# Kernel optimization log

Hardware: AMD Instinct MI355X
Metric: run time of the kernel (lower is better)

The kernel has to match this reference:

```python
import jax, jax.numpy as jnp
import numpy as np

H = 16  # heads

def setup_inputs() -> dict:
    key = jax.random.key(0)
    k1, k2, k3 = jax.random.split(key, 3)
    B, N, D = 2, 2048, 1024
    x = jax.random.normal(k1, (B, N, D), dtype=jnp.float32)
    W1 = jax.random.normal(k2, (D, 3 * D), dtype=jnp.float32) * (1.0 / np.sqrt(D))
    b1 = jnp.zeros((3 * D,), dtype=jnp.float32)
    W2 = jax.random.normal(k3, (D, D), dtype=jnp.float32) * (1.0 / np.sqrt(D))
    b2 = jnp.zeros((D,), dtype=jnp.float32)
    return {"x": x, "W1": W1, "b1": b1, "W2": W2, "b2": b2}

def reference(x, W1, b1, W2, b2):
    B, N, D = x.shape
    Dh = D // H  # head dim
    qkv = x @ W1 + b1                         # [B,N,3D]
    q, k, v = jnp.split(qkv, 3, axis=-1)
    q = q.reshape(B, N, H, Dh).transpose(0, 2, 1, 3)  # [B,H,N,Dh]
    k = k.reshape(B, N, H, Dh).transpose(0, 2, 1, 3)
    v = v.reshape(B, N, H, Dh).transpose(0, 2, 1, 3)
    scale = 1.0 / np.sqrt(Dh)
    w = jnp.einsum('bhnd,bhmd->bhnm', q, k) * scale   # [B,H,N,N]
    w = jax.nn.softmax(w, axis=-1)
    out = jnp.einsum('bhnm,bhmd->bhnd', w, v)         # [B,H,N,Dh]
    out = out.transpose(0, 2, 1, 3).reshape(B, N, D)
    return out @ W2 + b2
```

## Files before the change

kernel.cpp:

```cpp
#include <hip/hip_runtime.h>
#include <hip/hip_bf16.h>
#include <stdint.h>

#define B_   2
#define H_   16
#define N_   2048
#define D_   1024
#define DH   64
#define MTOK 4096

#define LOG2E 1.44269504088896f

typedef __attribute__((ext_vector_type(8)))  short bf16x8;
typedef __attribute__((ext_vector_type(4)))  float f32x4;
typedef __attribute__((ext_vector_type(16))) float f32x16;
typedef __attribute__((ext_vector_type(2)))  unsigned u32x2;
typedef __attribute__((ext_vector_type(4)))  unsigned short us4;

#define VMCNT_ASM(N) asm volatile("s_waitcnt vmcnt(" #N ")" ::: "memory")

static __device__ __forceinline__ unsigned short f2bf(float f) {
    union { float f; unsigned u; } v; v.f = f;
    unsigned r = v.u + 0x7fffu + ((v.u >> 16) & 1u);
    return (unsigned short)(r >> 16);
}

static __device__ __forceinline__ unsigned f2u(float x) {
    union { float f; unsigned u; } v; v.f = x; return v.u;
}
static __device__ __forceinline__ float u2f(unsigned x) {
    union { unsigned u; float f; } v; v.u = x; return v.f;
}

static __device__ __forceinline__ unsigned cvt_pk_bf16(float lo, float hi) {
    unsigned r;
    asm("v_cvt_pk_bf16_f32 %0, %1, %2" : "=v"(r) : "v"(lo), "v"(hi));
    return r;
}

static __device__ __forceinline__ bf16x8 frag_from_u32(unsigned a, unsigned b, unsigned c, unsigned d) {
    union { unsigned u[4]; bf16x8 v; } x;
    x.u[0] = a; x.u[1] = b; x.u[2] = c; x.u[3] = d;
    return x.v;
}

static __device__ __forceinline__ void load_lds16(const void* g, void* l) {
    __builtin_amdgcn_global_load_lds(
        (const __attribute__((address_space(1))) unsigned int*)g,
        (__attribute__((address_space(3))) unsigned int*)l, 16, 0, 0);
}

__global__ __launch_bounds__(256) void k_pre(const float* __restrict__ x,
                                             unsigned short* __restrict__ xb,
                                             const float* __restrict__ W1,
                                             unsigned short* __restrict__ w1t,
                                             const float* __restrict__ W2,
                                             unsigned short* __restrict__ w2t) {
    int blk = blockIdx.x;
    int t = threadIdx.x;
    if (blk < 4096) {
        int idx = (blk * 256 + t) * 4;
        float4 v = *(const float4*)(x + idx);
        us4 o;
        o.x = f2bf(v.x); o.y = f2bf(v.y); o.z = f2bf(v.z); o.w = f2bf(v.w);
        *(us4*)(xb + idx) = o;
        return;
    }
    const float* in;
    unsigned short* out;
    int C, bx, by;
    if (blk < 4864) { in = W1; out = w1t; C = 3072; int b2 = blk - 4096; bx = b2 % 48; by = b2 / 48; }
    else            { in = W2; out = w2t; C = 1024; int b2 = blk - 4864; bx = b2 % 16; by = b2 / 16; }
    const int R = 1024;
    __shared__ float tile[64][65];
    int c0 = bx * 64, r0 = by * 64;
    int tr = t >> 4, tc = (t & 15) * 4;
#pragma unroll
    for (int p = 0; p < 4; p++) {
        int row = p * 16 + tr;
        float4 v = *(const float4*)(in + (size_t)(r0 + row) * C + c0 + tc);
        tile[row][tc + 0] = v.x; tile[row][tc + 1] = v.y;
        tile[row][tc + 2] = v.z; tile[row][tc + 3] = v.w;
    }
    __syncthreads();
    int oc = t >> 4, orr = (t & 15) * 4;
#pragma unroll
    for (int p = 0; p < 4; p++) {
        int crow = p * 16 + oc;
        us4 o;
        o.x = f2bf(tile[orr + 0][crow]);
        o.y = f2bf(tile[orr + 1][crow]);
        o.z = f2bf(tile[orr + 2][crow]);
        o.w = f2bf(tile[orr + 3][crow]);
        *(us4*)(out + (size_t)(c0 + crow) * R + r0 + orr) = o;
    }
}

__global__ __launch_bounds__(512, 2) void k_gemm0(const unsigned short* __restrict__ A,
                                                  const unsigned short* __restrict__ Bt,
                                                  const float* __restrict__ bias,
                                                  unsigned short* __restrict__ qdst,
                                                  unsigned short* __restrict__ kdst,
                                                  unsigned short* __restrict__ vdst) {
    __shared__ unsigned short lds[57344];
    const int K = 1024, NT = 16;
    int tid = threadIdx.x;
    int lane = tid & 63, wv = tid >> 6;
    int wm = wv >> 2, wn = wv & 3;
    int F = blockIdx.x;
    int L = (F & 7) * 32 + (F >> 3);
    int n0 = (L % 16) * 192;
    int m0 = (L / 16) * 256;

    f32x4 acc[8][3];
#pragma unroll
    for (int i = 0; i < 8; i++)
#pragma unroll
        for (int j = 0; j < 3; j++) {
            f32x4 z; z[0] = 0.f; z[1] = 0.f; z[2] = 0.f; z[3] = 0.f;
            acc[i][j] = z;
        }

    auto stage = [&](int t) {
        int p = t & 1;
        int k0 = t * 64;
        unsigned short* ab = &lds[p * 16384];
        unsigned short* bb = &lds[32768 + p * 12288];
#pragma unroll
        for (int i = 0; i < 4; i++) {
            int u = i * 512 + tid;
            int r = u >> 3, c8 = u & 7;
            int c8s = c8 ^ (r & 7);
            int db = (i * 512 + wv * 64) * 8;
            load_lds16(A + (size_t)(m0 + r) * K + k0 + c8s * 8, &ab[db]);
            if (i < 3)
                load_lds16(Bt + (size_t)(n0 + r) * K + k0 + c8s * 8, &bb[db]);
        }
    };

    stage(0);
    stage(1);

    const int ml = lane & 15, ul = lane >> 4;
    bf16x8 afr[4], bfr[3];

#pragma unroll 1
    for (int t = 0; t < NT; ++t) {
        if (t < NT - 1) { VMCNT_ASM(7); }
        else            { VMCNT_ASM(0); }
        __builtin_amdgcn_s_barrier();

        const unsigned short* ab = &lds[(t & 1) * 16384];
        const unsigned short* bb = &lds[32768 + (t & 1) * 12288];

#pragma unroll
        for (int kk = 0; kk < 2; ++kk) {
            int ck = ((kk * 4 + ul) ^ (ml & 7)) * 8;
#pragma unroll
            for (int mh = 0; mh < 2; ++mh) {
                if (mh == 0) {
#pragma unroll
                    for (int nj = 0; nj < 3; nj++)
                        bfr[nj] = *(const bf16x8*)&bb[(wn * 48 + nj * 16 + ml) * 64 + ck];
                }
#pragma unroll
                for (int q = 0; q < 4; q++)
                    afr[q] = *(const bf16x8*)&ab[(wm * 128 + (mh * 4 + q) * 16 + ml) * 64 + ck];
                __builtin_amdgcn_s_barrier();
                __builtin_amdgcn_s_setprio(1);
#pragma unroll
                for (int q = 0; q < 4; q++)
#pragma unroll
                    for (int nj = 0; nj < 3; nj++)
                        acc[mh * 4 + q][nj] = __builtin_amdgcn_mfma_f32_16x16x32_bf16(
                            afr[q], bfr[nj], acc[mh * 4 + q][nj], 0, 0, 0);
                __builtin_amdgcn_s_setprio(0);
                __builtin_amdgcn_s_barrier();
            }
        }
        if (t + 2 < NT) stage(t + 2);
    }

#pragma unroll
    for (int nj = 0; nj < 3; nj++) {
        int col = n0 + wn * 48 + nj * 16 + (lane & 15);
        float bv = bias[col];
        int which = col >> 10;
        int hd = (col >> 6) & 15;
        int dh = col & 63;
        float scl = (which == 0) ? (0.125f * LOG2E) : 1.0f;
#pragma unroll
        for (int mi = 0; mi < 8; mi++) {
            int rbase = m0 + wm * 128 + mi * 16 + (lane >> 4) * 4;
#pragma unroll
            for (int r = 0; r < 4; r++) {
                int tok = rbase + r;
                int bb2 = tok >> 11, nn = tok & 2047;
                float vvv = (acc[mi][nj][r] + bv) * scl;
                size_t chunk = ((size_t)(bb2 * H_ + hd) * 64 + (nn >> 5)) * 2048;
                if (which == 0) {
                    qdst[((size_t)(bb2 * H_ + hd) * N_ + nn) * DH + dh] = f2bf(vvv);
                } else if (which == 1) {
                    int lane2 = ((dh >> 3) & 1) * 32 + (nn & 31);
                    kdst[chunk + (dh >> 4) * 512 + lane2 * 8 + (dh & 7)] = f2bf(vvv);
                } else {
                    int lane2 = ((nn >> 3) & 1) * 32 + (dh & 31);
                    int islot = (dh >> 5) * 2 + ((nn >> 4) & 1);
                    vdst[chunk + islot * 512 + lane2 * 8 + (nn & 7)] = f2bf(vvv);
                }
            }
        }
    }
}

__global__ __launch_bounds__(512, 2) void k_gemm1(const unsigned short* __restrict__ A,
                                                  const unsigned short* __restrict__ Bt,
                                                  const float* __restrict__ bias,
                                                  float* __restrict__ outp) {
    __shared__ unsigned short lds1[32768];
    const int K = 1024, NT = 16;
    int tid = threadIdx.x;
    int lane = tid & 63, wv = tid >> 6;
    int wm = wv >> 2, wn = wv & 3;
    int F = blockIdx.x;
    int L = (F & 7) * 32 + (F >> 3);
    int n0 = (L % 8) * 128;
    int m0 = (L / 8) * 128;
    int bIdx = m0 >> 11;
    int ntok0 = m0 & 2047;

    f32x4 acc[4][2];
#pragma unroll
    for (int i = 0; i < 4; i++)
#pragma unroll
        for (int j = 0; j < 2; j++) {
            f32x4 z; z[0] = 0.f; z[1] = 0.f; z[2] = 0.f; z[3] = 0.f;
            acc[i][j] = z;
        }

    auto stage = [&](int t) {
        int p = t & 1;
        const unsigned short* aptr = A + ((size_t)(bIdx * H_ + t) * N_ + ntok0) * DH;
        const unsigned short* bptr = Bt + (size_t)n0 * K + t * 64;
        unsigned short* ab = &lds1[p * 8192];
        unsigned short* bb = &lds1[16384 + p * 8192];
#pragma unroll
        for (int i = 0; i < 2; i++) {
            int u = i * 512 + tid;
            int r = u >> 3, c8 = u & 7;
            int c8s = c8 ^ (r & 7);
            int db = (i * 512 + wv * 64) * 8;
            load_lds16(aptr + (size_t)r * DH + c8s * 8, &ab[db]);
            load_lds16(bptr + (size_t)r * K  + c8s * 8, &bb[db]);
        }
    };

    stage(0);
    stage(1);

    const int ml = lane & 15, ul = lane >> 4;
    bf16x8 afr[4], bfr[2];

#pragma unroll 1
    for (int t = 0; t < NT; ++t) {
        if (t < NT - 1) { VMCNT_ASM(4); }
        else            { VMCNT_ASM(0); }
        __builtin_amdgcn_s_barrier();

        const unsigned short* ab = &lds1[(t & 1) * 8192];
        const unsigned short* bb = &lds1[16384 + (t & 1) * 8192];

#pragma unroll
        for (int kk = 0; kk < 2; ++kk) {
            int ck = ((kk * 4 + ul) ^ (ml & 7)) * 8;
#pragma unroll
            for (int nj = 0; nj < 2; nj++)
                bfr[nj] = *(const bf16x8*)&bb[(wn * 32 + nj * 16 + ml) * 64 + ck];
#pragma unroll
            for (int q = 0; q < 4; q++)
                afr[q] = *(const bf16x8*)&ab[(wm * 64 + q * 16 + ml) * 64 + ck];
            __builtin_amdgcn_s_barrier();
            __builtin_amdgcn_s_setprio(1);
#pragma unroll
            for (int q = 0; q < 4; q++)
#pragma unroll
                for (int nj = 0; nj < 2; nj++)
                    acc[q][nj] = __builtin_amdgcn_mfma_f32_16x16x32_bf16(
                        afr[q], bfr[nj], acc[q][nj], 0, 0, 0);
            __builtin_amdgcn_s_setprio(0);
            __builtin_amdgcn_s_barrier();
        }
        if (t + 2 < NT) stage(t + 2);
    }

#pragma unroll
    for (int nj = 0; nj < 2; nj++) {
        int col = n0 + wn * 32 + nj * 16 + ml;
        float bv = bias[col];
#pragma unroll
        for (int mi = 0; mi < 4; mi++) {
            int rbase = m0 + wm * 64 + mi * 16 + (lane >> 4) * 4;
#pragma unroll
            for (int r = 0; r < 4; r++)
                outp[(size_t)(rbase + r) * D_ + col] = acc[mi][nj][r] + bv;
        }
    }
}

__global__ __launch_bounds__(512, 2) void k_attn(const unsigned short* __restrict__ qh,
                                                 const unsigned short* __restrict__ ks,
                                                 const unsigned short* __restrict__ vs,
                                                 unsigned short* __restrict__ o) {
    __shared__ unsigned short smem[40960];
    unsigned short* kb = smem;
    unsigned short* vb = smem + 16384;
    float* red = (float*)smem;

    int tid = threadIdx.x;
    int lane = tid & 63, wv = tid >> 6;
    int qsub = wv >> 1;
    int kvh  = wv & 1;
    int F = blockIdx.x;
    int L = (F & 7) * 64 + (F >> 3);
    int bh = L >> 4;
    int q0 = (L & 15) * 128 + qsub * 32;
    int ln = lane & 31, hi = lane >> 5;
    const size_t bhO = (size_t)bh * N_ * DH;

    const unsigned short* qp = qh + bhO;
    bf16x8 qf[4];
#pragma unroll
    for (int kk = 0; kk < 4; kk++)
        qf[kk] = *(const bf16x8*)(qp + (size_t)(q0 + ln) * DH + kk * 16 + hi * 8);

    const unsigned short* kg = ks + (size_t)bh * 131072;
    const unsigned short* vg = vs + (size_t)bh * 131072;

    int sbuf = wv >> 1;
    int sl   = wv & 1;
    int sh   = sbuf & 1;
    const unsigned short* srcb = ((sbuf >> 1) ? vg : kg) + (size_t)sh * 65536 + sl * 2048;
    auto stageT = [&](int kr, int vr, int t) {
        unsigned short* dstb = (sbuf >> 1)
            ? vb + (vr * 2 + sh) * 4096 + sl * 2048
            : kb + (kr * 2 + sh) * 4096 + sl * 2048;
#pragma unroll
        for (int i = 0; i < 4; i++)
            load_lds16(srcb + (size_t)t * 4096 + i * 512 + lane * 8, dstb + i * 512);
    };

    f32x16 o0, o1;
#pragma unroll
    for (int r = 0; r < 16; r++) { o0[r] = 0.f; o1[r] = 0.f; }
    float m = -INFINITY, l = 0.f;

    auto softmax_pv = [&](const f32x16& sa, const f32x16& sb, const unsigned short* vB) {
        float mx[8];
#pragma unroll
        for (int i = 0; i < 8; i++)
            mx[i] = fmaxf(fmaxf(sa[i], sa[i + 8]), fmaxf(sb[i], sb[i + 8]));
#pragma unroll
        for (int i = 0; i < 4; i++) mx[i] = fmaxf(mx[i], mx[i + 4]);
        float mt = fmaxf(fmaxf(mx[0], mx[2]), fmaxf(mx[1], mx[3]));
        {
            u32x2 sw = __builtin_amdgcn_permlane32_swap(f2u(mt), f2u(mt), false, false);
            mt = fmaxf(u2f(sw[0]), u2f(sw[1]));
        }
        if (!__all(mt <= m + 8.0f)) {
            float mn = fmaxf(m, mt);
            float fs = __builtin_amdgcn_exp2f(m - mn);
            m = mn;
            l *= fs;
#pragma unroll
            for (int r = 0; r < 16; r++) { o0[r] *= fs; o1[r] *= fs; }
        }
        float pa[16], pb[16];
#pragma unroll
        for (int r = 0; r < 16; r++) {
            pa[r] = __builtin_amdgcn_exp2f(sa[r] - m);
            pb[r] = __builtin_amdgcn_exp2f(sb[r] - m);
        }
        float sm[8];
#pragma unroll
        for (int i = 0; i < 8; i++) sm[i] = (pa[i] + pa[i + 8]) + (pb[i] + pb[i + 8]);
#pragma unroll
        for (int i = 0; i < 4; i++) sm[i] = sm[i] + sm[i + 4];
        float sum = (sm[0] + sm[2]) + (sm[1] + sm[3]);
        {
            u32x2 sw = __builtin_amdgcn_permlane32_swap(f2u(sum), f2u(sum), false, false);
            sum = u2f(sw[0]) + u2f(sw[1]);
        }
        l += sum;

        unsigned pka[8], pkb[8];
#pragma unroll
        for (int i = 0; i < 8; i++) {
            pka[i] = cvt_pk_bf16(pa[2 * i], pa[2 * i + 1]);
            pkb[i] = cvt_pk_bf16(pb[2 * i], pb[2 * i + 1]);
        }
        u32x2 s0 = __builtin_amdgcn_permlane32_swap(pka[0], pka[2], false, false);
        u32x2 s1 = __builtin_amdgcn_permlane32_swap(pka[1], pka[3], false, false);
        u32x2 s2 = __builtin_amdgcn_permlane32_swap(pka[4], pka[6], false, false);
        u32x2 s3 = __builtin_amdgcn_permlane32_swap(pka[5], pka[7], false, false);
        bf16x8 pf0 = frag_from_u32(s0[0], s1[0], s0[1], s1[1]);
        bf16x8 pf1 = frag_from_u32(s2[0], s3[0], s2[1], s3[1]);
        s0 = __builtin_amdgcn_permlane32_swap(pkb[0], pkb[2], false, false);
        s1 = __builtin_amdgcn_permlane32_swap(pkb[1], pkb[3], false, false);
        s2 = __builtin_amdgcn_permlane32_swap(pkb[4], pkb[6], false, false);
        s3 = __builtin_amdgcn_permlane32_swap(pkb[5], pkb[7], false, false);
        bf16x8 pf2 = frag_from_u32(s0[0], s1[0], s0[1], s1[1]);
        bf16x8 pf3 = frag_from_u32(s2[0], s3[0], s2[1], s3[1]);

        bf16x8 vf0, vf1, vf2, vf3;
        vf0 = *(const bf16x8*)&vB[0 * 512 + lane * 8];
        vf1 = *(const bf16x8*)&vB[1 * 512 + lane * 8];
        vf2 = *(const bf16x8*)&vB[2048 + 0 * 512 + lane * 8];
        vf3 = *(const bf16x8*)&vB[2048 + 1 * 512 + lane * 8];
        o0 = __builtin_amdgcn_mfma_f32_32x32x16_bf16(vf0, pf0, o0, 0, 0, 0);
        o0 = __builtin_amdgcn_mfma_f32_32x32x16_bf16(vf1, pf1, o0, 0, 0, 0);
        o0 = __builtin_amdgcn_mfma_f32_32x32x16_bf16(vf2, pf2, o0, 0, 0, 0);
        o0 = __builtin_amdgcn_mfma_f32_32x32x16_bf16(vf3, pf3, o0, 0, 0, 0);
        vf0 = *(const bf16x8*)&vB[2 * 512 + lane * 8];
        vf1 = *(const bf16x8*)&vB[3 * 512 + lane * 8];
        vf2 = *(const bf16x8*)&vB[2048 + 2 * 512 + lane * 8];
        vf3 = *(const bf16x8*)&vB[2048 + 3 * 512 + lane * 8];
        o1 = __builtin_amdgcn_mfma_f32_32x32x16_bf16(vf0, pf0, o1, 0, 0, 0);
        o1 = __builtin_amdgcn_mfma_f32_32x32x16_bf16(vf1, pf1, o1, 0, 0, 0);
        o1 = __builtin_amdgcn_mfma_f32_32x32x16_bf16(vf2, pf2, o1, 0, 0, 0);
        o1 = __builtin_amdgcn_mfma_f32_32x32x16_bf16(vf3, pf3, o1, 0, 0, 0);
    };

    stageT(0, 0, 0);
    __syncthreads();

    f32x16 sa, sb;
#pragma unroll 1
    for (int t = 0; t < 16; ++t) {
        if (t < 15) stageT((t + 1) & 1, (t + 1) % 3, t + 1);

        if (t > 0) softmax_pv(sa, sb, vb + (((t - 1) % 3) * 2 + kvh) * 4096);

        const unsigned short* kB = kb + ((t & 1) * 2 + kvh) * 4096;
        bf16x8 kfa[4], kfb[4];
#pragma unroll
        for (int i = 0; i < 4; i++) {
            kfa[i] = *(const bf16x8*)&kB[i * 512 + lane * 8];
            kfb[i] = *(const bf16x8*)&kB[2048 + i * 512 + lane * 8];
        }
#pragma unroll
        for (int r = 0; r < 16; r++) { sa[r] = 0.f; sb[r] = 0.f; }
#pragma unroll
        for (int i = 0; i < 4; i++)
            sa = __builtin_amdgcn_mfma_f32_32x32x16_bf16(kfa[i], qf[i], sa, 0, 0, 0);
#pragma unroll
        for (int i = 0; i < 4; i++)
            sb = __builtin_amdgcn_mfma_f32_32x32x16_bf16(kfb[i], qf[i], sb, 0, 0, 0);

        __syncthreads();
    }
    softmax_pv(sa, sb, vb + (0 * 2 + kvh) * 4096);
    __syncthreads();

    if (kvh == 1) {
        float* rp = red + (qsub * 64 + lane) * 34;
#pragma unroll
        for (int r = 0; r < 16; r++) { rp[r] = o0[r]; rp[16 + r] = o1[r]; }
        rp[32] = m;
        rp[33] = l;
    }
    __syncthreads();
    if (kvh == 0) {
        const float* rp = red + (qsub * 64 + lane) * 34;
        float mb = rp[32], lb = rp[33];
        float mn = fmaxf(m, mb);
        float fa = __builtin_amdgcn_exp2f(m - mn);
        float fb = __builtin_amdgcn_exp2f(mb - mn);
        float inv = 1.0f / (l * fa + lb * fb);
        float ga = fa * inv, gb = fb * inv;
        unsigned short* ob = o + bhO + (size_t)(q0 + ln) * DH;
#pragma unroll
        for (int t2 = 0; t2 < 2; t2++) {
#pragma unroll
            for (int g = 0; g < 4; g++) {
                int d = t2 * 32 + g * 8 + hi * 4;
                int rb = g * 4;
                float a0 = (t2 ? o1[rb + 0] : o0[rb + 0]) * ga + rp[t2 * 16 + rb + 0] * gb;
                float a1 = (t2 ? o1[rb + 1] : o0[rb + 1]) * ga + rp[t2 * 16 + rb + 1] * gb;
                float a2 = (t2 ? o1[rb + 2] : o0[rb + 2]) * ga + rp[t2 * 16 + rb + 2] * gb;
                float a3 = (t2 ? o1[rb + 3] : o0[rb + 3]) * ga + rp[t2 * 16 + rb + 3] * gb;
                us4 w;
                w.x = f2bf(a0); w.y = f2bf(a1); w.z = f2bf(a2); w.w = f2bf(a3);
                *(us4*)(ob + d) = w;
            }
        }
    }
}

extern "C" void kernel_launch(void* const* d_in, const int* in_sizes, int n_in,
                              void* d_out, int out_size, void* d_ws, size_t ws_size,
                              hipStream_t stream) {
    const float* x  = (const float*)d_in[0];
    const float* W1 = (const float*)d_in[1];
    const float* b1 = (const float*)d_in[2];
    const float* W2 = (const float*)d_in[3];
    const float* b2 = (const float*)d_in[4];
    float* out = (float*)d_out;

    char* ws = (char*)d_ws;
    unsigned short* xb   = (unsigned short*)(ws);
    unsigned short* w1t  = (unsigned short*)(ws + 8388608);
    unsigned short* w2t  = (unsigned short*)(ws + 14680064);
    unsigned short* qh   = (unsigned short*)(ws + 16777216);
    unsigned short* ks   = (unsigned short*)(ws + 25165824);
    unsigned short* vsb  = (unsigned short*)(ws + 33554432);
    unsigned short* attn = (unsigned short*)(ws + 41943040);

    k_pre<<<5120, 256, 0, stream>>>(x, xb, W1, w1t, W2, w2t);
    k_gemm0<<<256, 512, 0, stream>>>(xb, w1t, b1, qh, ks, vsb);
    k_attn<<<512, 512, 0, stream>>>(qh, ks, vsb, attn);
    k_gemm1<<<256, 512, 0, stream>>>(attn, w2t, b2, out);
}
```

Measured before the change: 110.2 us.

## Shrink attention blocks to 256 threads with 32-key tiles and double buffering

The attention kernel now runs 1024 blocks of 256 threads, each covering 64 queries, instead of 512 blocks of 512 threads covering 128 queries. Each iteration processes a 32-key tile per wave instead of 64 and drops the software pipelining that deferred softmax/PV by one step. The K/V ring also goes from triple to double buffering, cutting LDS use. The aim is higher occupancy with less shared memory per block, at the cost of twice as many iterations and barriers and K/V traffic doubling across blocks.

```diff
diff --git a/kernel.cpp b/kernel.cpp
--- a/kernel.cpp
+++ b/kernel.cpp
@@ -307,13 +307,13 @@
     }
 }
 
-__global__ __launch_bounds__(512, 2) void k_attn(const unsigned short* __restrict__ qh,
+__global__ __launch_bounds__(256, 4) void k_attn(const unsigned short* __restrict__ qh,
                                                  const unsigned short* __restrict__ ks,
                                                  const unsigned short* __restrict__ vs,
                                                  unsigned short* __restrict__ o) {
-    __shared__ unsigned short smem[40960];
+    __shared__ unsigned short smem[16384];
     unsigned short* kb = smem;
-    unsigned short* vb = smem + 16384;
+    unsigned short* vb = smem + 8192;
     float* red = (float*)smem;
 
     int tid = threadIdx.x;
@@ -321,9 +321,9 @@
     int qsub = wv >> 1;
     int kvh  = wv & 1;
     int F = blockIdx.x;
-    int L = (F & 7) * 64 + (F >> 3);
-    int bh = L >> 4;
-    int q0 = (L & 15) * 128 + qsub * 32;
+    int L = (F & 7) * 128 + (F >> 3);
+    int bh = L >> 5;
+    int q0 = (L & 31) * 64 + qsub * 32;
     int ln = lane & 31, hi = lane >> 5;
     const size_t bhO = (size_t)bh * N_ * DH;
 
@@ -336,17 +336,14 @@
     const unsigned short* kg = ks + (size_t)bh * 131072;
     const unsigned short* vg = vs + (size_t)bh * 131072;
 
-    int sbuf = wv >> 1;
-    int sl   = wv & 1;
-    int sh   = sbuf & 1;
-    const unsigned short* srcb = ((sbuf >> 1) ? vg : kg) + (size_t)sh * 65536 + sl * 2048;
-    auto stageT = [&](int kr, int vr, int t) {
-        unsigned short* dstb = (sbuf >> 1)
-            ? vb + (vr * 2 + sh) * 4096 + sl * 2048
-            : kb + (kr * 2 + sh) * 4096 + sl * 2048;
+    int sh = wv & 1;
+    unsigned short* dstb = ((wv >> 1) ? vb : kb) + sh * 4096;
+    const unsigned short* srcb = ((wv >> 1) ? vg : kg) + (size_t)sh * 65536;
+    auto stageT = [&](int ring, int t) {
 #pragma unroll
         for (int i = 0; i < 4; i++)
-            load_lds16(srcb + (size_t)t * 4096 + i * 512 + lane * 8, dstb + i * 512);
+            load_lds16(srcb + (size_t)t * 2048 + i * 512 + lane * 8,
+                       dstb + ring * 2048 + i * 512);
     };
 
     f32x16 o0, o1;
@@ -354,11 +351,31 @@
     for (int r = 0; r < 16; r++) { o0[r] = 0.f; o1[r] = 0.f; }
     float m = -INFINITY, l = 0.f;
 
-    auto softmax_pv = [&](const f32x16& sa, const f32x16& sb, const unsigned short* vB) {
+    stageT(0, 0);
+    __syncthreads();
+
+#pragma unroll 1
+    for (int t = 0; t < 32; ++t) {
+        int b = t & 1;
+        if (t < 31) stageT(b ^ 1, t + 1);
+
+        const unsigned short* kB = kb + kvh * 4096 + b * 2048;
+        const unsigned short* vB = vb + kvh * 4096 + b * 2048;
+
+        bf16x8 kf[4];
+#pragma unroll
+        for (int i = 0; i < 4; i++)
+            kf[i] = *(const bf16x8*)&kB[i * 512 + lane * 8];
+        f32x16 s;
+#pragma unroll
+        for (int r = 0; r < 16; r++) s[r] = 0.f;
+#pragma unroll
+        for (int i = 0; i < 4; i++)
+            s = __builtin_amdgcn_mfma_f32_32x32x16_bf16(kf[i], qf[i], s, 0, 0, 0);
+
         float mx[8];
 #pragma unroll
-        for (int i = 0; i < 8; i++)
-            mx[i] = fmaxf(fmaxf(sa[i], sa[i + 8]), fmaxf(sb[i], sb[i + 8]));
+        for (int i = 0; i < 8; i++) mx[i] = fmaxf(s[i], s[i + 8]);
 #pragma unroll
         for (int i = 0; i < 4; i++) mx[i] = fmaxf(mx[i], mx[i + 4]);
         float mt = fmaxf(fmaxf(mx[0], mx[2]), fmaxf(mx[1], mx[3]));
@@ -374,15 +391,12 @@
 #pragma unroll
             for (int r = 0; r < 16; r++) { o0[r] *= fs; o1[r] *= fs; }
         }
-        float pa[16], pb[16];
-#pragma unroll
-        for (int r = 0; r < 16; r++) {
-            pa[r] = __builtin_amdgcn_exp2f(sa[r] - m);
-            pb[r] = __builtin_amdgcn_exp2f(sb[r] - m);
-        }
+        float p[16];
+#pragma unroll
+        for (int r = 0; r < 16; r++) p[r] = __builtin_amdgcn_exp2f(s[r] - m);
         float sm[8];
 #pragma unroll
-        for (int i = 0; i < 8; i++) sm[i] = (pa[i] + pa[i + 8]) + (pb[i] + pb[i + 8]);
+        for (int i = 0; i < 8; i++) sm[i] = p[i] + p[i + 8];
 #pragma unroll
         for (int i = 0; i < 4; i++) sm[i] = sm[i] + sm[i + 4];
         float sum = (sm[0] + sm[2]) + (sm[1] + sm[3]);
@@ -392,74 +406,27 @@
         }
         l += sum;
 
-        unsigned pka[8], pkb[8];
-#pragma unroll
-        for (int i = 0; i < 8; i++) {
-            pka[i] = cvt_pk_bf16(pa[2 * i], pa[2 * i + 1]);
-            pkb[i] = cvt_pk_bf16(pb[2 * i], pb[2 * i + 1]);
-        }
-        u32x2 s0 = __builtin_amdgcn_permlane32_swap(pka[0], pka[2], false, false);
-        u32x2 s1 = __builtin_amdgcn_permlane32_swap(pka[1], pka[3], false, false);
-        u32x2 s2 = __builtin_amdgcn_permlane32_swap(pka[4], pka[6], false, false);
-        u32x2 s3 = __builtin_amdgcn_permlane32_swap(pka[5], pka[7], false, false);
+        unsigned pk[8];
+#pragma unroll
+        for (int i = 0; i < 8; i++) pk[i] = cvt_pk_bf16(p[2 * i], p[2 * i + 1]);
+        u32x2 s0 = __builtin_amdgcn_permlane32_swap(pk[0], pk[2], false, false);
+        u32x2 s1 = __builtin_amdgcn_permlane32_swap(pk[1], pk[3], false, false);
+        u32x2 s2 = __builtin_amdgcn_permlane32_swap(pk[4], pk[6], false, false);
+        u32x2 s3 = __builtin_amdgcn_permlane32_swap(pk[5], pk[7], false, false);
         bf16x8 pf0 = frag_from_u32(s0[0], s1[0], s0[1], s1[1]);
         bf16x8 pf1 = frag_from_u32(s2[0], s3[0], s2[1], s3[1]);
-        s0 = __builtin_amdgcn_permlane32_swap(pkb[0], pkb[2], false, false);
-        s1 = __builtin_amdgcn_permlane32_swap(pkb[1], pkb[3], false, false);
-        s2 = __builtin_amdgcn_permlane32_swap(pkb[4], pkb[6], false, false);
-        s3 = __builtin_amdgcn_permlane32_swap(pkb[5], pkb[7], false, false);
-        bf16x8 pf2 = frag_from_u32(s0[0], s1[0], s0[1], s1[1]);
-        bf16x8 pf3 = frag_from_u32(s2[0], s3[0], s2[1], s3[1]);
-
-        bf16x8 vf0, vf1, vf2, vf3;
-        vf0 = *(const bf16x8*)&vB[0 * 512 + lane * 8];
-        vf1 = *(const bf16x8*)&vB[1 * 512 + lane * 8];
-        vf2 = *(const bf16x8*)&vB[2048 + 0 * 512 + lane * 8];
-        vf3 = *(const bf16x8*)&vB[2048 + 1 * 512 + lane * 8];
+
+        bf16x8 vf0 = *(const bf16x8*)&vB[0 * 512 + lane * 8];
+        bf16x8 vf1 = *(const bf16x8*)&vB[1 * 512 + lane * 8];
+        bf16x8 vf2 = *(const bf16x8*)&vB[2 * 512 + lane * 8];
+        bf16x8 vf3 = *(const bf16x8*)&vB[3 * 512 + lane * 8];
         o0 = __builtin_amdgcn_mfma_f32_32x32x16_bf16(vf0, pf0, o0, 0, 0, 0);
         o0 = __builtin_amdgcn_mfma_f32_32x32x16_bf16(vf1, pf1, o0, 0, 0, 0);
-        o0 = __builtin_amdgcn_mfma_f32_32x32x16_bf16(vf2, pf2, o0, 0, 0, 0);
-        o0 = __builtin_amdgcn_mfma_f32_32x32x16_bf16(vf3, pf3, o0, 0, 0, 0);
-        vf0 = *(const bf16x8*)&vB[2 * 512 + lane * 8];
-        vf1 = *(const bf16x8*)&vB[3 * 512 + lane * 8];
-        vf2 = *(const bf16x8*)&vB[2048 + 2 * 512 + lane * 8];
-        vf3 = *(const bf16x8*)&vB[2048 + 3 * 512 + lane * 8];
-        o1 = __builtin_amdgcn_mfma_f32_32x32x16_bf16(vf0, pf0, o1, 0, 0, 0);
-        o1 = __builtin_amdgcn_mfma_f32_32x32x16_bf16(vf1, pf1, o1, 0, 0, 0);
-        o1 = __builtin_amdgcn_mfma_f32_32x32x16_bf16(vf2, pf2, o1, 0, 0, 0);
-        o1 = __builtin_amdgcn_mfma_f32_32x32x16_bf16(vf3, pf3, o1, 0, 0, 0);
-    };
-
-    stageT(0, 0, 0);
-    __syncthreads();
-
-    f32x16 sa, sb;
-#pragma unroll 1
-    for (int t = 0; t < 16; ++t) {
-        if (t < 15) stageT((t + 1) & 1, (t + 1) % 3, t + 1);
-
-        if (t > 0) softmax_pv(sa, sb, vb + (((t - 1) % 3) * 2 + kvh) * 4096);
-
-        const unsigned short* kB = kb + ((t & 1) * 2 + kvh) * 4096;
-        bf16x8 kfa[4], kfb[4];
-#pragma unroll
-        for (int i = 0; i < 4; i++) {
-            kfa[i] = *(const bf16x8*)&kB[i * 512 + lane * 8];
-            kfb[i] = *(const bf16x8*)&kB[2048 + i * 512 + lane * 8];
-        }
-#pragma unroll
-        for (int r = 0; r < 16; r++) { sa[r] = 0.f; sb[r] = 0.f; }
-#pragma unroll
-        for (int i = 0; i < 4; i++)
-            sa = __builtin_amdgcn_mfma_f32_32x32x16_bf16(kfa[i], qf[i], sa, 0, 0, 0);
-#pragma unroll
-        for (int i = 0; i < 4; i++)
-            sb = __builtin_amdgcn_mfma_f32_32x32x16_bf16(kfb[i], qf[i], sb, 0, 0, 0);
+        o1 = __builtin_amdgcn_mfma_f32_32x32x16_bf16(vf2, pf0, o1, 0, 0, 0);
+        o1 = __builtin_amdgcn_mfma_f32_32x32x16_bf16(vf3, pf1, o1, 0, 0, 0);
 
         __syncthreads();
     }
-    softmax_pv(sa, sb, vb + (0 * 2 + kvh) * 4096);
-    __syncthreads();
 
     if (kvh == 1) {
         float* rp = red + (qsub * 64 + lane) * 34;
@@ -517,6 +484,6 @@
 
     k_pre<<<5120, 256, 0, stream>>>(x, xb, W1, w1t, W2, w2t);
     k_gemm0<<<256, 512, 0, stream>>>(xb, w1t, b1, qh, ks, vsb);
-    k_attn<<<512, 512, 0, stream>>>(qh, ks, vsb, attn);
+    k_attn<<<1024, 256, 0, stream>>>(qh, ks, vsb, attn);
     k_gemm1<<<256, 512, 0, stream>>>(attn, w2t, b2, out);
 }
```

After: 116.0 us. +5.3%, slower.
